# Performance work log

Measured on AMD Instinct MI355X. Metric: run time of the kernel, lower is better.

The kernel has to match this reference:

```python
import jax, jax.numpy as jnp
import numpy as np
from jax import lax

C = 128
HEADS = 8
HID = 256  # int(C * 2.0)
B, H, W = 8, 128, 128
EPS_LN = 1e-5
EPS_NORM = 1e-12


def _dwconv(x, w, pad):
    # x: [B,C,H,W], w: [C,1,kh,kw] depthwise
    return lax.conv_general_dilated(
        x, w, window_strides=(1, 1), padding=[(pad, pad), (pad, pad)],
        dimension_numbers=("NCHW", "OIHW", "NCHW"), feature_group_count=x.shape[1])


def _conv1x1(x, w):
    # w: [O, I] pointwise conv
    return jnp.einsum("oi,bihw->bohw", w, x)


def _layernorm_c(x, gamma, beta):
    # torch: reshape to [B, HW, C], LayerNorm over C, reshape back == LN over channel axis
    mu = jnp.mean(x, axis=1, keepdims=True)
    var = jnp.mean(jnp.square(x - mu), axis=1, keepdims=True)
    xn = (x - mu) * lax.rsqrt(var + EPS_LN)
    return xn * gamma[None, :, None, None] + beta[None, :, None, None]


def _l2norm(x):
    n = jnp.sqrt(jnp.sum(jnp.square(x), axis=-1, keepdims=True))
    return x / jnp.maximum(n, EPS_NORM)


def _mdta(x, qkv_w, qkv_dw, temperature, attn_proj):
    b, c, h, w = x.shape
    qkv = _dwconv(_conv1x1(x, qkv_w), qkv_dw, pad=1)  # [B,3C,H,W]
    q, k, v = jnp.split(qkv, 3, axis=1)
    hd = c // HEADS
    q = q.reshape(b, HEADS, hd, h * w)
    k = k.reshape(b, HEADS, hd, h * w)
    v = v.reshape(b, HEADS, hd, h * w)
    q, k = _l2norm(q), _l2norm(k)
    attn = jax.nn.softmax(jnp.einsum("bhdn,bhen->bhde", q, k) * temperature, axis=-1)
    out = jnp.einsum("bhde,bhen->bhdn", attn, v).reshape(b, c, h, w)
    return _conv1x1(out, attn_proj)


def _gdfn2(x, pin_w, c1_w, c3_w, c5_w, pout_w):
    x = _conv1x1(x, pin_w)  # [B,HID,H,W]
    x1 = x * c1_w[None, :, 0, 0, 0, None, None]  # depthwise 1x1 == per-channel scale
    x3 = _dwconv(x, c3_w, pad=1)
    x5 = _dwconv(x, c5_w, pad=2)
    g = jax.nn.gelu(x1, approximate=False)
    gated = jnp.concatenate([g * x3, g * x5], axis=1)  # [B,2*HID,H,W]
    return _conv1x1(gated, pout_w)


def setup_inputs() -> dict:
    key = jax.random.key(0)
    ks = jax.random.split(key, 12)
    s = 0.05
    return {
        "x": jax.random.normal(ks[0], (B, C, H, W), jnp.float32),
        "ln1_w": jnp.ones((C,), jnp.float32),
        "ln1_b": jnp.zeros((C,), jnp.float32),
        "qkv_w": jax.random.normal(ks[1], (3 * C, C), jnp.float32) * s,
        "qkv_dw": jax.random.normal(ks[2], (3 * C, 1, 3, 3), jnp.float32) * s,
        "temperature": jnp.ones((1, HEADS, 1, 1), jnp.float32),
        "attn_proj": jax.random.normal(ks[3], (C, C), jnp.float32) * s,
        "ln2_w": jnp.ones((C,), jnp.float32),
        "ln2_b": jnp.zeros((C,), jnp.float32),
        "pin_w": jax.random.normal(ks[4], (HID, C), jnp.float32) * s,
        "c1_w": jax.random.normal(ks[5], (HID, 1, 1, 1), jnp.float32) * s,
        "c3_w": jax.random.normal(ks[6], (HID, 1, 3, 3), jnp.float32) * s,
        "c5_w": jax.random.normal(ks[7], (HID, 1, 5, 5), jnp.float32) * s,
        "pout_w": jax.random.normal(ks[8], (C, 2 * HID), jnp.float32) * s,
    }


def reference(x, ln1_w, ln1_b, qkv_w, qkv_dw, temperature, attn_proj,
              ln2_w, ln2_b, pin_w, c1_w, c3_w, c5_w, pout_w):
    x = x + _mdta(_layernorm_c(x, ln1_w, ln1_b), qkv_w, qkv_dw, temperature, attn_proj)
    x = x + _gdfn2(_layernorm_c(x, ln2_w, ln2_b), pin_w, c1_w, c3_w, c5_w, pout_w)
    return x
```

## Files before the change

kernel.cpp:

```cpp
#include <hip/hip_runtime.h>

typedef unsigned short ushort;
typedef unsigned int uint;
typedef __bf16 bf16x8 __attribute__((ext_vector_type(8)));
typedef unsigned short ushort8v __attribute__((ext_vector_type(8)));
typedef float f32x4 __attribute__((ext_vector_type(4)));

__device__ __forceinline__ float b2f(ushort u) {
    unsigned int x = ((unsigned int)u) << 16;
    float f;
    __builtin_memcpy(&f, &x, 4);
    return f;
}
__device__ __forceinline__ ushort f2bf(float f) {
    unsigned int x;
    __builtin_memcpy(&x, &f, 4);
    unsigned int r = x + 0x7fffu + ((x >> 16) & 1u);
    return (ushort)(r >> 16);
}
__device__ __forceinline__ float u2f_lo(uint u) {
    uint x = u << 16;
    float f;
    __builtin_memcpy(&f, &x, 4);
    return f;
}
__device__ __forceinline__ float u2f_hi(uint u) {
    uint x = u & 0xffff0000u;
    float f;
    __builtin_memcpy(&f, &x, 4);
    return f;
}
__device__ __forceinline__ uint packbf(float a, float b) {
    return (uint)f2bf(a) | ((uint)f2bf(b) << 16);
}
__device__ __forceinline__ ushort to_bf(float f) { return f2bf(f); }
__device__ __forceinline__ ushort to_bf(ushort u) { return u; }

#define NPIX 16384
#define PSTRIDE 136

__device__ __forceinline__ void stage_plane(ushort* pl, const ushort* __restrict__ src, int tid) {
    uint* plu = (uint*)pl;
    for (int i = tid; i < 784; i += 256) {
        int idx;
        if (i < 136) idx = i;
        else if (i < 272) idx = 8840 + (i - 136);
        else {
            int j = i - 272;
            int r = (j >> 2) + 2;
            int cs = j & 3;
            idx = r * 68 + (cs == 0 ? 0 : 64 + cs);
        }
        plu[idx] = 0u;
    }
    for (int i = tid; i < 2048; i += 256) {
        int row = i >> 4, xg = (i & 15) << 3;
        uint4 v = *(const uint4*)&src[row * 128 + xg];
        uint* dst = (uint*)&pl[(row + 2) * PSTRIDE + xg + 2];
        dst[0] = v.x; dst[1] = v.y; dst[2] = v.z; dst[3] = v.w;
    }
    __syncthreads();
}

__device__ __forceinline__ void unpack12(const ushort* rowp, float* cc) {
    const uint* rp = (const uint*)rowp;
    uint4 u = *(const uint4*)rp;
    uint2 v = *(const uint2*)(rp + 4);
    cc[0] = u2f_lo(u.x); cc[1] = u2f_hi(u.x);
    cc[2] = u2f_lo(u.y); cc[3] = u2f_hi(u.y);
    cc[4] = u2f_lo(u.z); cc[5] = u2f_hi(u.z);
    cc[6] = u2f_lo(u.w); cc[7] = u2f_hi(u.w);
    cc[8] = u2f_lo(v.x); cc[9] = u2f_hi(v.x);
    cc[10] = u2f_lo(v.y); cc[11] = u2f_hi(v.y);
}

__global__ __launch_bounds__(256) void wcvt(const float* __restrict__ s0, ushort* __restrict__ d0, int n0,
                                            const float* __restrict__ s1, ushort* __restrict__ d1, int n1,
                                            const float* __restrict__ s2, ushort* __restrict__ d2, int n2) {
    int i = blockIdx.x * 256 + threadIdx.x;
    if (i < n0) d0[i] = f2bf(s0[i]);
    else if (i < n0 + n1) d1[i - n0] = f2bf(s1[i - n0]);
    else if (i < n0 + n1 + n2) d2[i - n0 - n1] = f2bf(s2[i - n0 - n1]);
}

template <int O, typename TIN>
__global__ __launch_bounds__(256) void ln_gemm_mfma(const TIN* __restrict__ xin,
                                                    const ushort* __restrict__ Wb,
                                                    const float* __restrict__ gamma,
                                                    const float* __restrict__ beta,
                                                    ushort* __restrict__ out) {
    __shared__ ushort xs[64][136];
    __shared__ float red[2][4][64];
    __shared__ float mu[64], rs[64];
    __shared__ float gl[128], bl[128];

    const int blk = blockIdx.x;
    const int b = blk >> 8;
    const int pix0 = (blk & 255) * 64;
    const int tid = threadIdx.x;

    const TIN* xb = xin + (size_t)b * 128 * NPIX + pix0;
    for (int i = tid; i < 1024; i += 256) {
        int p = i & 63, cg = i >> 6;
        const TIN* src = xb + (size_t)(cg * 8) * NPIX + p;
        ushort8v u;
#pragma unroll
        for (int j = 0; j < 8; j++) u[j] = to_bf(src[(size_t)j * NPIX]);
        *(ushort8v*)&xs[p][cg * 8] = u;
    }
    if (tid < 128) {
        gl[tid] = gamma[tid];
        bl[tid] = beta[tid];
    }
    __syncthreads();

    {
        const int p = tid & 63, part = tid >> 6;
        float s = 0.f, ss = 0.f;
#pragma unroll
        for (int q = 0; q < 4; q++) {
            ushort8v u = *(const ushort8v*)&xs[p][part * 32 + q * 8];
#pragma unroll
            for (int j = 0; j < 8; j++) {
                float v = b2f(u[j]);
                s += v;
                ss += v * v;
            }
        }
        red[0][part][p] = s;
        red[1][part][p] = ss;
    }
    __syncthreads();
    if (tid < 64) {
        float s = red[0][0][tid] + red[0][1][tid] + red[0][2][tid] + red[0][3][tid];
        float ss = red[1][0][tid] + red[1][1][tid] + red[1][2][tid] + red[1][3][tid];
        float m = s * (1.f / 128.f);
        float var = ss * (1.f / 128.f) - m * m;
        mu[tid] = m;
        rs[tid] = rsqrtf(var + 1e-5f);
    }
    __syncthreads();
    {
        const int p = tid & 63, part = tid >> 6;
        const float mp = mu[p], rp = rs[p];
#pragma unroll
        for (int q = 0; q < 4; q++) {
            int c0 = part * 32 + q * 8;
            ushort8v u = *(const ushort8v*)&xs[p][c0];
            ushort8v o;
#pragma unroll
            for (int j = 0; j < 8; j++) {
                float v = b2f(u[j]);
                o[j] = f2bf((v - mp) * rp * gl[c0 + j] + bl[c0 + j]);
            }
            *(ushort8v*)&xs[p][c0] = o;
        }
    }
    __syncthreads();

    const int wv = tid >> 6, lane = tid & 63;
    const int lr = lane & 15, lg = lane >> 4;

    bf16x8 bfr[4][4];
#pragma unroll
    for (int t = 0; t < 4; t++)
#pragma unroll
        for (int kc = 0; kc < 4; kc++)
            bfr[t][kc] = __builtin_bit_cast(bf16x8, *(const ushort8v*)&xs[t * 16 + lr][kc * 32 + lg * 8]);

    constexpr int MT = O / 64;
#pragma unroll 1
    for (int mt = 0; mt < MT; mt++) {
        const int o0 = (wv * MT + mt) * 16;
        bf16x8 afr[4];
#pragma unroll
        for (int kc = 0; kc < 4; kc++)
            afr[kc] = __builtin_bit_cast(bf16x8,
                *(const ushort8v*)&Wb[(size_t)(o0 + lr) * 128 + kc * 32 + lg * 8]);
        f32x4 acc[4] = {{0.f, 0.f, 0.f, 0.f}, {0.f, 0.f, 0.f, 0.f}, {0.f, 0.f, 0.f, 0.f}, {0.f, 0.f, 0.f, 0.f}};
#pragma unroll
        for (int kc = 0; kc < 4; kc++)
#pragma unroll
            for (int t = 0; t < 4; t++)
                acc[t] = __builtin_amdgcn_mfma_f32_16x16x32_bf16(afr[kc], bfr[t][kc], acc[t], 0, 0, 0);
#pragma unroll
        for (int t = 0; t < 4; t++)
#pragma unroll
            for (int r = 0; r < 4; r++) {
                int o = o0 + lg * 4 + r;
                out[((size_t)b * O + o) * NPIX + pix0 + t * 16 + lr] = f2bf(acc[t][r]);
            }
    }
}

__global__ __launch_bounds__(256) void dwconv3_lds(const ushort* __restrict__ in,
                                                   const float* __restrict__ wdw,
                                                   ushort* __restrict__ out) {
    __shared__ ushort pl[132 * PSTRIDE];
    const int c = blockIdx.x;
    const size_t plane = ((size_t)blockIdx.y * gridDim.x + c) * NPIX;
    const int tid = threadIdx.x;

    float w[9];
#pragma unroll
    for (int j = 0; j < 9; j++) w[j] = wdw[c * 9 + j];

    stage_plane(pl, in + plane, tid);

    const int x = (tid & 15) * 8;
    const int ybase = tid >> 4;
#pragma unroll 1
    for (int k = 0; k < 8; k++) {
        const int y = k * 16 + ybase;
        float a[8];
#pragma unroll
        for (int p = 0; p < 8; p++) a[p] = 0.f;
#pragma unroll
        for (int ky = 0; ky < 3; ky++) {
            float cc[12];
            unpack12(&pl[(y + ky + 1) * PSTRIDE + x], cc);
#pragma unroll
            for (int kx = 0; kx < 3; kx++) {
                float wv = w[ky * 3 + kx];
#pragma unroll
                for (int p = 0; p < 8; p++) a[p] += cc[p + kx + 1] * wv;
            }
        }
        const int px0 = (y << 7) + x;
        uint4 o;
        o.x = packbf(a[0], a[1]);
        o.y = packbf(a[2], a[3]);
        o.z = packbf(a[4], a[5]);
        o.w = packbf(a[6], a[7]);
        *(uint4*)&out[plane + px0] = o;
    }
}

__global__ __launch_bounds__(256) void dw_gated(const ushort* __restrict__ t,
                                                const float* __restrict__ w3_,
                                                const float* __restrict__ w5_,
                                                const float* __restrict__ c1w,
                                                ushort* __restrict__ gated) {
    __shared__ ushort pl[132 * PSTRIDE];
    const int c = blockIdx.x;
    const int b = blockIdx.y;
    const int tid = threadIdx.x;

    float w3[9], w5[25];
#pragma unroll
    for (int j = 0; j < 9; j++) w3[j] = w3_[c * 9 + j];
#pragma unroll
    for (int j = 0; j < 25; j++) w5[j] = w5_[c * 25 + j];
    const float c1v = c1w[c];

    stage_plane(pl, t + ((size_t)b * 256 + c) * NPIX, tid);

    ushort* g3 = gated + ((size_t)b * 512 + c) * NPIX;
    ushort* g5 = g3 + (size_t)256 * NPIX;

    const int x = (tid & 15) * 8;
    const int ybase = tid >> 4;
#pragma unroll 1
    for (int k = 0; k < 8; k++) {
        const int y = k * 16 + ybase;
        float a5[8], a3[8], tc[8];
#pragma unroll
        for (int p = 0; p < 8; p++) { a5[p] = 0.f; a3[p] = 0.f; }
#pragma unroll
        for (int ky = 0; ky < 5; ky++) {
            float cc[12];
            unpack12(&pl[(y + ky) * PSTRIDE + x], cc);
#pragma unroll
            for (int kx = 0; kx < 5; kx++) {
                float wv = w5[ky * 5 + kx];
#pragma unroll
                for (int p = 0; p < 8; p++) a5[p] += cc[p + kx] * wv;
            }
            if (ky >= 1 && ky <= 3) {
#pragma unroll
                for (int kx = 0; kx < 3; kx++) {
                    float wv = w3[(ky - 1) * 3 + kx];
#pragma unroll
                    for (int p = 0; p < 8; p++) a3[p] += cc[p + kx + 1] * wv;
                }
            }
            if (ky == 2) {
#pragma unroll
                for (int p = 0; p < 8; p++) tc[p] = cc[p + 2];
            }
        }
        const int px0 = (y << 7) + x;
        uint4 o3, o5;
        float g[8];
#pragma unroll
        for (int p = 0; p < 8; p++) {
            float x1 = tc[p] * c1v;
            g[p] = x1 * __builtin_amdgcn_rcpf(1.f + __expf(-1.702f * x1));
        }
        o3.x = packbf(g[0] * a3[0], g[1] * a3[1]);
        o3.y = packbf(g[2] * a3[2], g[3] * a3[3]);
        o3.z = packbf(g[4] * a3[4], g[5] * a3[5]);
        o3.w = packbf(g[6] * a3[6], g[7] * a3[7]);
        o5.x = packbf(g[0] * a5[0], g[1] * a5[1]);
        o5.y = packbf(g[2] * a5[2], g[3] * a5[3]);
        o5.z = packbf(g[4] * a5[4], g[5] * a5[5]);
        o5.w = packbf(g[6] * a5[6], g[7] * a5[7]);
        *(uint4*)&g3[px0] = o3;
        *(uint4*)&g5[px0] = o5;
    }
}

__global__ __launch_bounds__(256) void attn_M(const ushort* __restrict__ qkv,
                                              const float* __restrict__ temp,
                                              const float* __restrict__ attn_proj,
                                              ushort* __restrict__ M) {
    __shared__ float Sp[4][16][16];
    __shared__ float QSS[4][16], KSS[4][16];
    __shared__ float A[16][17];

    const int bh = blockIdx.x, b = bh >> 3, h = bh & 7;
    const int tid = threadIdx.x;
    const int w = tid >> 6, lane = tid & 63;
    const int lr = lane & 15, lg = lane >> 4;

    const ushort* qrow = qkv + ((size_t)b * 384 + h * 16 + lr) * NPIX + w * 4096 + lg * 8;
    const ushort* krow = qkv + ((size_t)b * 384 + 128 + h * 16 + lr) * NPIX + w * 4096 + lg * 8;

    f32x4 acc = {0.f, 0.f, 0.f, 0.f};
    f32x4 accq = {0.f, 0.f, 0.f, 0.f};
    f32x4 acck = {0.f, 0.f, 0.f, 0.f};
#pragma unroll 2
    for (int it = 0; it < 128; it++) {
        bf16x8 qf = __builtin_bit_cast(bf16x8, *(const ushort8v*)(qrow + it * 32));
        bf16x8 kf = __builtin_bit_cast(bf16x8, *(const ushort8v*)(krow + it * 32));
        acc = __builtin_amdgcn_mfma_f32_16x16x32_bf16(qf, kf, acc, 0, 0, 0);
        accq = __builtin_amdgcn_mfma_f32_16x16x32_bf16(qf, qf, accq, 0, 0, 0);
        acck = __builtin_amdgcn_mfma_f32_16x16x32_bf16(kf, kf, acck, 0, 0, 0);
    }
#pragma unroll
    for (int r = 0; r < 4; r++) Sp[w][lg * 4 + r][lr] = acc[r];
    if (lg == (lr >> 2)) {
        QSS[w][lr] = accq[lr & 3];
        KSS[w][lr] = acck[lr & 3];
    }
    __syncthreads();

    const int d = tid >> 4, e = tid & 15;
    float S = Sp[0][d][e] + Sp[1][d][e] + Sp[2][d][e] + Sp[3][d][e];
    float nq = fmaxf(sqrtf(QSS[0][d] + QSS[1][d] + QSS[2][d] + QSS[3][d]), 1e-12f);
    float nk = fmaxf(sqrtf(KSS[0][e] + KSS[1][e] + KSS[2][e] + KSS[3][e]), 1e-12f);
    float logit = S / (nq * nk) * temp[h];
    float m = logit;
    for (int off = 8; off; off >>= 1) m = fmaxf(m, __shfl_xor(m, off, 64));
    float ex = expf(logit - m);
    float sum = ex;
    for (int off = 8; off; off >>= 1) sum += __shfl_xor(sum, off, 64);
    A[d][e] = ex / sum;
    __syncthreads();

    for (int i = tid; i < 2048; i += 256) {
        int o = i >> 4, ee = i & 15;
        float acc2 = 0.f;
#pragma unroll
        for (int dd = 0; dd < 16; dd++) acc2 += attn_proj[o * 128 + h * 16 + dd] * A[dd][ee];
        M[((size_t)b * 128 + o) * 128 + h * 16 + ee] = f2bf(acc2);
    }
}

__global__ __launch_bounds__(256) void mv_res_mfma(const ushort* __restrict__ qkv,
                                                   const ushort* __restrict__ Mb16,
                                                   const float* __restrict__ x,
                                                   ushort* __restrict__ x2) {
    __shared__ ushort vs[64][136];
    const int blk = blockIdx.x;
    const int b = blk >> 8;
    const int pix0 = (blk & 255) * 64;
    const int tid = threadIdx.x;

    const ushort* vb = qkv + ((size_t)b * 384 + 256) * NPIX + pix0;
    for (int i = tid; i < 1024; i += 256) {
        int p = i & 63, cg = i >> 6;
        const ushort* src = vb + (size_t)(cg * 8) * NPIX + p;
        ushort8v u;
#pragma unroll
        for (int j = 0; j < 8; j++) u[j] = src[(size_t)j * NPIX];
        *(ushort8v*)&vs[p][cg * 8] = u;
    }
    __syncthreads();

    const int wv = tid >> 6, lane = tid & 63;
    const int lr = lane & 15, lg = lane >> 4;

    bf16x8 bfr[4][4];
#pragma unroll
    for (int t = 0; t < 4; t++)
#pragma unroll
        for (int kc = 0; kc < 4; kc++)
            bfr[t][kc] = __builtin_bit_cast(bf16x8, *(const ushort8v*)&vs[t * 16 + lr][kc * 32 + lg * 8]);

    const ushort* Mb = Mb16 + (size_t)b * 128 * 128;
#pragma unroll 1
    for (int mt = 0; mt < 2; mt++) {
        const int o0 = (wv * 2 + mt) * 16;
        bf16x8 afr[4];
#pragma unroll
        for (int kc = 0; kc < 4; kc++)
            afr[kc] = __builtin_bit_cast(bf16x8,
                *(const ushort8v*)&Mb[(size_t)(o0 + lr) * 128 + kc * 32 + lg * 8]);
        f32x4 acc[4] = {{0.f, 0.f, 0.f, 0.f}, {0.f, 0.f, 0.f, 0.f}, {0.f, 0.f, 0.f, 0.f}, {0.f, 0.f, 0.f, 0.f}};
#pragma unroll
        for (int kc = 0; kc < 4; kc++)
#pragma unroll
            for (int t = 0; t < 4; t++)
                acc[t] = __builtin_amdgcn_mfma_f32_16x16x32_bf16(afr[kc], bfr[t][kc], acc[t], 0, 0, 0);
#pragma unroll
        for (int t = 0; t < 4; t++)
#pragma unroll
            for (int r = 0; r < 4; r++) {
                int o = o0 + lg * 4 + r;
                size_t off = ((size_t)b * 128 + o) * NPIX + pix0 + t * 16 + lr;
                x2[off] = f2bf(x[off] + acc[t][r]);
            }
    }
}

__global__ __launch_bounds__(256) void gdfn_mfma(const ushort* __restrict__ gated,
                                                 const ushort* __restrict__ x2,
                                                 const ushort* __restrict__ pout_b,
                                                 float* __restrict__ out) {
    __shared__ ushort gs[64][72];

    const int blk = blockIdx.x;
    const int b = blk >> 8;
    const int pix0 = (blk & 255) * 64;
    const int tid = threadIdx.x;
    const int wv = tid >> 6, lane = tid & 63;
    const int lr = lane & 15, lg = lane >> 4;

    f32x4 acc[2][4];
#pragma unroll
    for (int mt = 0; mt < 2; mt++)
#pragma unroll
        for (int tt = 0; tt < 4; tt++) acc[mt][tt] = (f32x4){0.f, 0.f, 0.f, 0.f};

#pragma unroll 1
    for (int kb = 0; kb < 8; kb++) {
        __syncthreads();
        for (int i = tid; i < 512; i += 256) {
            int p = i & 63, kg = i >> 6;
            const ushort* src = gated + ((size_t)b * 512 + kb * 64 + kg * 8) * NPIX + pix0 + p;
            ushort8v u;
#pragma unroll
            for (int j = 0; j < 8; j++) u[j] = src[(size_t)j * NPIX];
            *(ushort8v*)&gs[p][kg * 8] = u;
        }
        __syncthreads();

        bf16x8 bfrg[4][2];
#pragma unroll
        for (int tt = 0; tt < 4; tt++)
#pragma unroll
            for (int kc = 0; kc < 2; kc++)
                bfrg[tt][kc] = __builtin_bit_cast(bf16x8, *(const ushort8v*)&gs[tt * 16 + lr][kc * 32 + lg * 8]);

#pragma unroll
        for (int mt = 0; mt < 2; mt++) {
            const int o0 = (wv * 2 + mt) * 16;
            bf16x8 afr[2];
#pragma unroll
            for (int kc = 0; kc < 2; kc++)
                afr[kc] = __builtin_bit_cast(bf16x8,
                    *(const ushort8v*)&pout_b[(size_t)(o0 + lr) * 512 + kb * 64 + kc * 32 + lg * 8]);
#pragma unroll
            for (int kc = 0; kc < 2; kc++)
#pragma unroll
                for (int tt = 0; tt < 4; tt++)
                    acc[mt][tt] = __builtin_amdgcn_mfma_f32_16x16x32_bf16(afr[kc], bfrg[tt][kc], acc[mt][tt], 0, 0, 0);
        }
    }

#pragma unroll
    for (int mt = 0; mt < 2; mt++)
#pragma unroll
        for (int tt = 0; tt < 4; tt++)
#pragma unroll
            for (int r = 0; r < 4; r++) {
                int o = (wv * 2 + mt) * 16 + lg * 4 + r;
                size_t off = ((size_t)b * 128 + o) * NPIX + pix0 + tt * 16 + lr;
                out[off] = b2f(x2[off]) + acc[mt][tt][r];
            }
}

extern "C" void kernel_launch(void* const* d_in, const int* in_sizes, int n_in,
                              void* d_out, int out_size, void* d_ws, size_t ws_size,
                              hipStream_t stream) {
    const float* x = (const float*)d_in[0];
    const float* ln1_w = (const float*)d_in[1];
    const float* ln1_b = (const float*)d_in[2];
    const float* qkv_w = (const float*)d_in[3];
    const float* qkv_dw = (const float*)d_in[4];
    const float* temperature = (const float*)d_in[5];
    const float* attn_proj = (const float*)d_in[6];
    const float* ln2_w = (const float*)d_in[7];
    const float* ln2_b = (const float*)d_in[8];
    const float* pin_w = (const float*)d_in[9];
    const float* c1_w = (const float*)d_in[10];
    const float* c3_w = (const float*)d_in[11];
    const float* c5_w = (const float*)d_in[12];
    const float* pout_w = (const float*)d_in[13];
    float* out = (float*)d_out;

    char* ws = (char*)d_ws;
    ushort* qkv_pre = (ushort*)(ws + 0);
    ushort* qkv     = (ushort*)(ws + 100663296);
    ushort* x2      = (ushort*)(ws + 201326592);
    ushort* t       = (ushort*)(ws + 0);
    ushort* gated   = (ushort*)(ws + 67108864);
    ushort* Mb16    = (ushort*)(ws + 235151360);
    ushort* qkv_wb  = (ushort*)(ws + 235413504);
    ushort* pin_wb  = (ushort*)(ws + 235511808);
    ushort* pout_wb = (ushort*)(ws + 235577344);

    wcvt<<<576, 256, 0, stream>>>(qkv_w, qkv_wb, 49152, pin_w, pin_wb, 32768, pout_w, pout_wb, 65536);
    ln_gemm_mfma<384, float><<<2048, 256, 0, stream>>>(x, qkv_wb, ln1_w, ln1_b, qkv_pre);
    dwconv3_lds<<<dim3(384, 8), 256, 0, stream>>>(qkv_pre, qkv_dw, qkv);
    attn_M<<<64, 256, 0, stream>>>(qkv, temperature, attn_proj, Mb16);
    mv_res_mfma<<<2048, 256, 0, stream>>>(qkv, Mb16, x, x2);
    ln_gemm_mfma<256, ushort><<<2048, 256, 0, stream>>>(x2, pin_wb, ln2_w, ln2_b, t);
    dw_gated<<<dim3(256, 8), 256, 0, stream>>>(t, c3_w, c5_w, c1_w, gated);
    gdfn_mfma<<<2048, 256, 0, stream>>>(gated, x2, pout_wb, out);
}
```

Before: 337.9 us.

## Store intermediates in pixel-tiled channel-blocked layout for contiguous tile access

Intermediate bf16 buffers (qkv_pre, qkv, x2, t, gated) switch from NCHW planes to a [B][tile of 64 pixels][C][64] layout. GEMM kernels that gather a 64-pixel tile across all channels then read one contiguous block instead of strided rows from each plane, which should improve coalescing and DRAM locality. The depthwise conv kernels now read and write in 128-byte chunks scattered across tiles, and attn_M's sequential reads stride by 384*64 elements, so those kernels may lose locality.

```diff
diff --git a/kernel.cpp b/kernel.cpp
--- a/kernel.cpp
+++ b/kernel.cpp
@@ -1,4 +1,5 @@
 #include <hip/hip_runtime.h>
+#include <type_traits>
 
 typedef unsigned short ushort;
 typedef unsigned int uint;
@@ -33,13 +34,16 @@
 __device__ __forceinline__ uint packbf(float a, float b) {
     return (uint)f2bf(a) | ((uint)f2bf(b) << 16);
 }
-__device__ __forceinline__ ushort to_bf(float f) { return f2bf(f); }
-__device__ __forceinline__ ushort to_bf(ushort u) { return u; }
 
 #define NPIX 16384
 #define PSTRIDE 136
 
-__device__ __forceinline__ void stage_plane(ushort* pl, const ushort* __restrict__ src, int tid) {
+__device__ __forceinline__ size_t tadr(int b, int CH, int tile, int ch, int off) {
+    return (((size_t)b * 256 + tile) * CH + ch) * 64 + off;
+}
+
+__device__ __forceinline__ void stage_plane(ushort* pl, const ushort* __restrict__ src,
+                                            int b, int c, int CH, int tid) {
     uint* plu = (uint*)pl;
     for (int i = tid; i < 784; i += 256) {
         int idx;
@@ -55,7 +59,8 @@
     }
     for (int i = tid; i < 2048; i += 256) {
         int row = i >> 4, xg = (i & 15) << 3;
-        uint4 v = *(const uint4*)&src[row * 128 + xg];
+        int px0 = row * 128 + xg;
+        uint4 v = *(const uint4*)&src[tadr(b, CH, px0 >> 6, c, px0 & 63)];
         uint* dst = (uint*)&pl[(row + 2) * PSTRIDE + xg + 2];
         dst[0] = v.x; dst[1] = v.y; dst[2] = v.z; dst[3] = v.w;
     }
@@ -96,17 +101,28 @@
 
     const int blk = blockIdx.x;
     const int b = blk >> 8;
-    const int pix0 = (blk & 255) * 64;
+    const int tile = blk & 255;
     const int tid = threadIdx.x;
 
-    const TIN* xb = xin + (size_t)b * 128 * NPIX + pix0;
-    for (int i = tid; i < 1024; i += 256) {
-        int p = i & 63, cg = i >> 6;
-        const TIN* src = xb + (size_t)(cg * 8) * NPIX + p;
-        ushort8v u;
-#pragma unroll
-        for (int j = 0; j < 8; j++) u[j] = to_bf(src[(size_t)j * NPIX]);
-        *(ushort8v*)&xs[p][cg * 8] = u;
+    if constexpr (std::is_same<TIN, float>::value) {
+        const float* xb = xin + (size_t)b * 128 * NPIX + tile * 64;
+        for (int i = tid; i < 1024; i += 256) {
+            int p = i & 63, cg = i >> 6;
+            const float* src = xb + (size_t)(cg * 8) * NPIX + p;
+            ushort8v u;
+#pragma unroll
+            for (int j = 0; j < 8; j++) u[j] = f2bf(src[(size_t)j * NPIX]);
+            *(ushort8v*)&xs[p][cg * 8] = u;
+        }
+    } else {
+        const ushort* xb = xin + tadr(b, 128, tile, 0, 0);
+        for (int i = tid; i < 1024; i += 256) {
+            int p = i & 63, cg = i >> 6;
+            ushort8v u;
+#pragma unroll
+            for (int j = 0; j < 8; j++) u[j] = xb[(cg * 8 + j) * 64 + p];
+            *(ushort8v*)&xs[p][cg * 8] = u;
+        }
     }
     if (tid < 128) {
         gl[tid] = gamma[tid];
@@ -188,24 +204,24 @@
 #pragma unroll
             for (int r = 0; r < 4; r++) {
                 int o = o0 + lg * 4 + r;
-                out[((size_t)b * O + o) * NPIX + pix0 + t * 16 + lr] = f2bf(acc[t][r]);
+                out[tadr(b, O, tile, o, t * 16 + lr)] = f2bf(acc[t][r]);
             }
     }
 }
 
 __global__ __launch_bounds__(256) void dwconv3_lds(const ushort* __restrict__ in,
                                                    const float* __restrict__ wdw,
-                                                   ushort* __restrict__ out) {
+                                                   ushort* __restrict__ out, int CH) {
     __shared__ ushort pl[132 * PSTRIDE];
     const int c = blockIdx.x;
-    const size_t plane = ((size_t)blockIdx.y * gridDim.x + c) * NPIX;
+    const int b = blockIdx.y;
     const int tid = threadIdx.x;
 
     float w[9];
 #pragma unroll
     for (int j = 0; j < 9; j++) w[j] = wdw[c * 9 + j];
 
-    stage_plane(pl, in + plane, tid);
+    stage_plane(pl, in, b, c, CH, tid);
 
     const int x = (tid & 15) * 8;
     const int ybase = tid >> 4;
@@ -232,7 +248,7 @@
         o.y = packbf(a[2], a[3]);
         o.z = packbf(a[4], a[5]);
         o.w = packbf(a[6], a[7]);
-        *(uint4*)&out[plane + px0] = o;
+        *(uint4*)&out[tadr(b, CH, px0 >> 6, c, px0 & 63)] = o;
     }
 }
 
@@ -253,10 +269,7 @@
     for (int j = 0; j < 25; j++) w5[j] = w5_[c * 25 + j];
     const float c1v = c1w[c];
 
-    stage_plane(pl, t + ((size_t)b * 256 + c) * NPIX, tid);
-
-    ushort* g3 = gated + ((size_t)b * 512 + c) * NPIX;
-    ushort* g5 = g3 + (size_t)256 * NPIX;
+    stage_plane(pl, t, b, c, 256, tid);
 
     const int x = (tid & 15) * 8;
     const int ybase = tid >> 4;
@@ -305,8 +318,8 @@
         o5.y = packbf(g[2] * a5[2], g[3] * a5[3]);
         o5.z = packbf(g[4] * a5[4], g[5] * a5[5]);
         o5.w = packbf(g[6] * a5[6], g[7] * a5[7]);
-        *(uint4*)&g3[px0] = o3;
-        *(uint4*)&g5[px0] = o5;
+        *(uint4*)&gated[tadr(b, 512, px0 >> 6, c, px0 & 63)] = o3;
+        *(uint4*)&gated[tadr(b, 512, px0 >> 6, 256 + c, px0 & 63)] = o5;
     }
 }
 
@@ -323,16 +336,17 @@
     const int w = tid >> 6, lane = tid & 63;
     const int lr = lane & 15, lg = lane >> 4;
 
-    const ushort* qrow = qkv + ((size_t)b * 384 + h * 16 + lr) * NPIX + w * 4096 + lg * 8;
-    const ushort* krow = qkv + ((size_t)b * 384 + 128 + h * 16 + lr) * NPIX + w * 4096 + lg * 8;
+    const size_t qbase = (((size_t)b * 256 + w * 64) * 384 + h * 16 + lr) * 64 + lg * 8;
+    const size_t kbase = qbase + (size_t)128 * 64;
 
     f32x4 acc = {0.f, 0.f, 0.f, 0.f};
     f32x4 accq = {0.f, 0.f, 0.f, 0.f};
     f32x4 acck = {0.f, 0.f, 0.f, 0.f};
 #pragma unroll 2
     for (int it = 0; it < 128; it++) {
-        bf16x8 qf = __builtin_bit_cast(bf16x8, *(const ushort8v*)(qrow + it * 32));
-        bf16x8 kf = __builtin_bit_cast(bf16x8, *(const ushort8v*)(krow + it * 32));
+        size_t off = (size_t)(it >> 1) * (384 * 64) + (it & 1) * 32;
+        bf16x8 qf = __builtin_bit_cast(bf16x8, *(const ushort8v*)(qkv + qbase + off));
+        bf16x8 kf = __builtin_bit_cast(bf16x8, *(const ushort8v*)(qkv + kbase + off));
         acc = __builtin_amdgcn_mfma_f32_16x16x32_bf16(qf, kf, acc, 0, 0, 0);
         accq = __builtin_amdgcn_mfma_f32_16x16x32_bf16(qf, qf, accq, 0, 0, 0);
         acck = __builtin_amdgcn_mfma_f32_16x16x32_bf16(kf, kf, acck, 0, 0, 0);
@@ -374,16 +388,15 @@
     __shared__ ushort vs[64][136];
     const int blk = blockIdx.x;
     const int b = blk >> 8;
-    const int pix0 = (blk & 255) * 64;
+    const int tile = blk & 255;
     const int tid = threadIdx.x;
 
-    const ushort* vb = qkv + ((size_t)b * 384 + 256) * NPIX + pix0;
+    const ushort* vb = qkv + tadr(b, 384, tile, 256, 0);
     for (int i = tid; i < 1024; i += 256) {
         int p = i & 63, cg = i >> 6;
-        const ushort* src = vb + (size_t)(cg * 8) * NPIX + p;
         ushort8v u;
 #pragma unroll
-        for (int j = 0; j < 8; j++) u[j] = src[(size_t)j * NPIX];
+        for (int j = 0; j < 8; j++) u[j] = vb[(cg * 8 + j) * 64 + p];
         *(ushort8v*)&vs[p][cg * 8] = u;
     }
     __syncthreads();
@@ -418,8 +431,8 @@
 #pragma unroll
             for (int r = 0; r < 4; r++) {
                 int o = o0 + lg * 4 + r;
-                size_t off = ((size_t)b * 128 + o) * NPIX + pix0 + t * 16 + lr;
-                x2[off] = f2bf(x[off] + acc[t][r]);
+                float xv = x[((size_t)b * 128 + o) * NPIX + tile * 64 + t * 16 + lr];
+                x2[tadr(b, 128, tile, o, t * 16 + lr)] = f2bf(xv + acc[t][r]);
             }
     }
 }
@@ -432,10 +445,12 @@
 
     const int blk = blockIdx.x;
     const int b = blk >> 8;
-    const int pix0 = (blk & 255) * 64;
+    const int tile = blk & 255;
     const int tid = threadIdx.x;
     const int wv = tid >> 6, lane = tid & 63;
     const int lr = lane & 15, lg = lane >> 4;
+
+    const ushort* gb = gated + tadr(b, 512, tile, 0, 0);
 
     f32x4 acc[2][4];
 #pragma unroll
@@ -448,10 +463,10 @@
         __syncthreads();
         for (int i = tid; i < 512; i += 256) {
             int p = i & 63, kg = i >> 6;
-            const ushort* src = gated + ((size_t)b * 512 + kb * 64 + kg * 8) * NPIX + pix0 + p;
+            const ushort* src = gb + (kb * 64 + kg * 8) * 64 + p;
             ushort8v u;
 #pragma unroll
-            for (int j = 0; j < 8; j++) u[j] = src[(size_t)j * NPIX];
+            for (int j = 0; j < 8; j++) u[j] = src[j * 64];
             *(ushort8v*)&gs[p][kg * 8] = u;
         }
         __syncthreads();
@@ -486,8 +501,8 @@
 #pragma unroll
             for (int r = 0; r < 4; r++) {
                 int o = (wv * 2 + mt) * 16 + lg * 4 + r;
-                size_t off = ((size_t)b * 128 + o) * NPIX + pix0 + tt * 16 + lr;
-                out[off] = b2f(x2[off]) + acc[mt][tt][r];
+                float xv = b2f(x2[tadr(b, 128, tile, o, tt * 16 + lr)]);
+                out[((size_t)b * 128 + o) * NPIX + tile * 64 + tt * 16 + lr] = xv + acc[mt][tt][r];
             }
 }
 
@@ -523,7 +538,7 @@
 
     wcvt<<<576, 256, 0, stream>>>(qkv_w, qkv_wb, 49152, pin_w, pin_wb, 32768, pout_w, pout_wb, 65536);
     ln_gemm_mfma<384, float><<<2048, 256, 0, stream>>>(x, qkv_wb, ln1_w, ln1_b, qkv_pre);
-    dwconv3_lds<<<dim3(384, 8), 256, 0, stream>>>(qkv_pre, qkv_dw, qkv);
+    dwconv3_lds<<<dim3(384, 8), 256, 0, stream>>>(qkv_pre, qkv_dw, qkv, 384);
     attn_M<<<64, 256, 0, stream>>>(qkv, temperature, attn_proj, Mb16);
     mv_res_mfma<<<2048, 256, 0, stream>>>(qkv, Mb16, x, x2);
     ln_gemm_mfma<256, ushort><<<2048, 256, 0, stream>>>(x2, pin_wb, ln2_w, ln2_b, t);
```

New measurement: 324.8 us. -3.9%, faster.
